# Performance work log

Measured on AMD Instinct MI355X. Metric: run time of the kernel, lower is better.

## Reference

```python
import jax, jax.numpy as jnp
import numpy as np

LN_EPS = 1e-5


def setup_inputs() -> dict:
    key = jax.random.key(0)
    ks = jax.random.split(key, 6)
    B, T, D, E, F = 8, 2048, 1024, 8, 4096
    x = jax.random.normal(ks[0], (B, T, D), dtype=jnp.float32)
    router_w = jax.random.normal(ks[1], (E, D), dtype=jnp.float32) * 0.02
    wfc = jax.random.normal(ks[2], (E, F, D), dtype=jnp.float32) * 0.02
    bfc = jnp.zeros((E, F), dtype=jnp.float32)
    wproj = jax.random.normal(ks[3], (E, D, F), dtype=jnp.float32) * 0.02
    bproj = jnp.zeros((E, D), dtype=jnp.float32)
    ln_g = jnp.ones((D,), dtype=jnp.float32)
    ln_b = jnp.zeros((D,), dtype=jnp.float32)
    return {"x": x, "router_w": router_w, "wfc": wfc, "bfc": bfc,
            "wproj": wproj, "bproj": bproj, "ln_g": ln_g, "ln_b": ln_b,
            "top_k": 2}


def reference(x, router_w, wfc, bfc, wproj, bproj, ln_g, ln_b, top_k):
    # Router: [B,T,E] logits, top-k selection, softmax over the k logits.
    router_logits = jnp.einsum('btd,ed->bte', x, router_w)
    top_vals, top_idx = jax.lax.top_k(router_logits, top_k)   # [B,T,K]
    top_probs = jax.nn.softmax(top_vals, axis=-1)             # [B,T,K]

    E = router_w.shape[0]
    out = jnp.zeros_like(x)
    # Dense-per-expert compute with zero gate for unrouted tokens; identical
    # math to the torch gather/scatter loop (dropout inert in eval).
    for e in range(E):
        gate = jnp.sum(jnp.where(top_idx == e, top_probs, 0.0), axis=-1)  # [B,T]
        h = jax.nn.gelu(jnp.einsum('btd,fd->btf', x, wfc[e]) + bfc[e],
                        approximate=False)
        y = jnp.einsum('btf,df->btd', h, wproj[e]) + bproj[e]
        out = out + y * gate[..., None]

    # LayerNorm over hidden dim
    mu = jnp.mean(out, axis=-1, keepdims=True)
    var = jnp.mean(jnp.square(out - mu), axis=-1, keepdims=True)
    out = (out - mu) * jax.lax.rsqrt(var + LN_EPS) * ln_g + ln_b
    return (out, router_logits)
```

## Files before the change

### kernel.cpp

```cpp
#include <hip/hip_runtime.h>

#define NTOK 16384
#define DDIM 1024
#define FDIM 4096
#define NEXP 8
#define PADPAIRS 33792
#define MAXTILES 264

#define WS_XB      0ull
#define WS_WFCB    33554432ull
#define WS_WPROJB  100663296ull
#define WS_H       167772160ull

typedef short bf16x8 __attribute__((ext_vector_type(8)));
typedef float f32x4 __attribute__((ext_vector_type(4)));

__device__ __forceinline__ unsigned short f2bf(float f) {
    unsigned int u = __float_as_uint(f);
    u += 0x7fffu + ((u >> 16) & 1u);
    return (unsigned short)(u >> 16);
}

__device__ __forceinline__ void gload16(const unsigned short* g, const unsigned short* lds) {
    __builtin_amdgcn_global_load_lds(
        (const __attribute__((address_space(1))) unsigned int*)(unsigned long long)(const void*)g,
        (__attribute__((address_space(3))) unsigned int*)(unsigned int)(unsigned long long)(const void*)lds,
        16, 0, 0);
}

__global__ __launch_bounds__(256) void convert_kernel(const float* __restrict__ src,
                                                      unsigned short* __restrict__ dst) {
    int i = blockIdx.x * 256 + threadIdx.x;
    float4 v = ((const float4*)src)[i];
    ushort4 o;
    o.x = f2bf(v.x); o.y = f2bf(v.y); o.z = f2bf(v.z); o.w = f2bf(v.w);
    ((ushort4*)dst)[i] = o;
}

__global__ __launch_bounds__(256) void router_kernel(const float* __restrict__ x,
                                                     const float* __restrict__ rw,
                                                     unsigned short* __restrict__ xb,
                                                     float* __restrict__ logits,
                                                     int* __restrict__ tok_idx,
                                                     float* __restrict__ tok_gate,
                                                     int* __restrict__ counts) {
    __shared__ float srw[NEXP * DDIM];
    __shared__ int scnt[NEXP];
    int tid = threadIdx.x;
    if (tid < NEXP) scnt[tid] = 0;
    for (int i = tid; i < NEXP * DDIM / 4; i += 256)
        ((float4*)srw)[i] = ((const float4*)rw)[i];
    __syncthreads();

    int wave = tid >> 6, lane = tid & 63;
    const float4* srw4 = (const float4*)srw;

    for (int j = 0; j < 4; j++) {
        int t = blockIdx.x * 16 + wave * 4 + j;
        const float4* xr = (const float4*)(x + (size_t)t * DDIM);
        ushort4* xbr = (ushort4*)(xb + (size_t)t * DDIM);

        float acc[NEXP];
#pragma unroll
        for (int e = 0; e < NEXP; e++) acc[e] = 0.f;

#pragma unroll
        for (int i = 0; i < 4; i++) {
            int k4 = i * 64 + lane;
            float4 xv = xr[k4];
            ushort4 o;
            o.x = f2bf(xv.x); o.y = f2bf(xv.y); o.z = f2bf(xv.z); o.w = f2bf(xv.w);
            xbr[k4] = o;
#pragma unroll
            for (int e = 0; e < NEXP; e++) {
                float4 wv = srw4[e * 256 + k4];
                acc[e] += xv.x * wv.x + xv.y * wv.y + xv.z * wv.z + xv.w * wv.w;
            }
        }
#pragma unroll
        for (int off = 1; off < 64; off <<= 1) {
#pragma unroll
            for (int e = 0; e < NEXP; e++) acc[e] += __shfl_xor(acc[e], off);
        }
        if (lane == 0) {
            float v0 = -1e30f, v1 = -1e30f; int i0 = 0, i1 = 0;
#pragma unroll
            for (int e = 0; e < NEXP; e++) {
                float v = acc[e];
                logits[(size_t)t * NEXP + e] = v;
                if (v > v0)      { v1 = v0; i1 = i0; v0 = v; i0 = e; }
                else if (v > v1) { v1 = v;  i1 = e; }
            }
            float d = __expf(v1 - v0);
            float g0 = 1.f / (1.f + d);
            float g1 = d * g0;
            tok_idx[t * 2 + 0] = i0; tok_idx[t * 2 + 1] = i1;
            tok_gate[t * 2 + 0] = g0; tok_gate[t * 2 + 1] = g1;
            atomicAdd(&scnt[i0], 1);
            atomicAdd(&scnt[i1], 1);
        }
    }
    __syncthreads();
    if (tid < NEXP) atomicAdd(&counts[tid], scnt[tid]);
}

__global__ void seg_plan(const int* __restrict__ counts, int* __restrict__ seg_start,
                         int* __restrict__ tile2e, int* __restrict__ total_tiles,
                         int* __restrict__ pair_token, float* __restrict__ pair_gate) {
    if (threadIdx.x == 0) {
        int cum = 0, tl = 0;
        for (int e = 0; e < NEXP; e++) {
            seg_start[e] = cum;
            int tiles = (counts[e] + 127) >> 7;
            for (int i = 0; i < tiles; i++) tile2e[tl++] = e;
            cum += tiles << 7;
        }
        for (int i = tl; i < MAXTILES; i++) tile2e[i] = -1;
        *total_tiles = tl;
    }
    for (int i = threadIdx.x; i < PADPAIRS; i += 256) {
        pair_token[i] = 0;
        pair_gate[i] = 0.f;
    }
}

__global__ __launch_bounds__(256) void scatter_k(const int* __restrict__ tok_idx,
                                                 const float* __restrict__ tok_gate,
                                                 const int* __restrict__ seg_start,
                                                 int* __restrict__ cursor,
                                                 int* __restrict__ pair_token,
                                                 float* __restrict__ pair_gate) {
    int t = blockIdx.x * 256 + threadIdx.x;
#pragma unroll
    for (int s = 0; s < 2; s++) {
        int e = tok_idx[t * 2 + s];
        int pos = seg_start[e] + atomicAdd(&cursor[e], 1);
        pair_token[pos] = t;
        pair_gate[pos] = tok_gate[t * 2 + s];
    }
}

__global__ __launch_bounds__(256, 3) void gemm1_kernel(const unsigned short* __restrict__ xb,
                                                    const unsigned short* __restrict__ wfcb,
                                                    const float* __restrict__ bfc,
                                                    const int* __restrict__ pair_token,
                                                    const int* __restrict__ tile2e,
                                                    int chunk_base,
                                                    unsigned short* __restrict__ h) {
    int tile = chunk_base + blockIdx.y;
    int e = tile2e[tile];
    if (e < 0) return;
    int ftile = blockIdx.x;

    __shared__ unsigned short sA[128 * 64];
    __shared__ unsigned short sB[128 * 64];

    int tid = threadIdx.x;
    int wave = tid >> 6, lane = tid & 63;
    int lrow = lane >> 3;
    int kblk = (lane & 7) ^ lrow;

    const unsigned short* wB = wfcb + (size_t)e * FDIM * DDIM + (size_t)ftile * 128 * DDIM;
    const unsigned short* aBase[4];
    const unsigned short* bBase[4];
#pragma unroll
    for (int t = 0; t < 4; t++) {
        int row = wave * 32 + t * 8 + lrow;
        aBase[t] = xb + (size_t)pair_token[tile * 128 + row] * DDIM + kblk * 8;
        bBase[t] = wB + (size_t)row * DDIM + kblk * 8;
    }

    f32x4 zero = {0.f, 0.f, 0.f, 0.f};
    f32x4 acc[4][4];
#pragma unroll
    for (int i = 0; i < 4; i++)
#pragma unroll
        for (int j = 0; j < 4; j++) acc[i][j] = zero;

    int wm = (wave >> 1) * 64, wn = (wave & 1) * 64;
    int quad = lane >> 4, l16 = lane & 15;
    int r7 = l16 & 7;

    for (int k0 = 0; k0 < DDIM; k0 += 64) {
#pragma unroll
        for (int t = 0; t < 4; t++) {
            gload16(aBase[t], &sA[(wave * 32 + t * 8) * 64]);
            gload16(bBase[t], &sB[(wave * 32 + t * 8) * 64]);
            aBase[t] += 64; bBase[t] += 64;
        }
        __syncthreads();
#pragma unroll
        for (int ks = 0; ks < 64; ks += 32) {
            int g = (ks >> 3) + quad;
            bf16x8 af[4], bfr[4];
#pragma unroll
            for (int i = 0; i < 4; i++) {
                int row = wm + i * 16 + l16;
                af[i] = *(const bf16x8*)&sA[row * 64 + ((g ^ r7) << 3)];
            }
#pragma unroll
            for (int j = 0; j < 4; j++) {
                int row = wn + j * 16 + l16;
                bfr[j] = *(const bf16x8*)&sB[row * 64 + ((g ^ r7) << 3)];
            }
#pragma unroll
            for (int i = 0; i < 4; i++)
#pragma unroll
                for (int j = 0; j < 4; j++)
                    acc[i][j] = __builtin_amdgcn_mfma_f32_16x16x32_bf16(af[i], bfr[j], acc[i][j], 0, 0, 0);
        }
        __syncthreads();
    }

    unsigned short* hrow_base = h + (size_t)blockIdx.y * 128 * FDIM;
#pragma unroll
    for (int i = 0; i < 4; i++) {
#pragma unroll
        for (int j = 0; j < 4; j++) {
            int col = wn + j * 16 + l16;
            int f = ftile * 128 + col;
            float bias = bfc[e * FDIM + f];
#pragma unroll
            for (int r = 0; r < 4; r++) {
                int row = wm + i * 16 + quad * 4 + r;
                float v = acc[i][j][r] + bias;
                v = 0.5f * v * (1.f + erff(v * 0.70710678118654752f));
                hrow_base[(size_t)row * FDIM + f] = f2bf(v);
            }
        }
    }
}

__global__ __launch_bounds__(256, 3) void gemm2_kernel(const unsigned short* __restrict__ h,
                                                    const unsigned short* __restrict__ wprojb,
                                                    const float* __restrict__ bproj,
                                                    const int* __restrict__ pair_token,
                                                    const float* __restrict__ pair_gate,
                                                    const int* __restrict__ tile2e,
                                                    int chunk_base,
                                                    float* __restrict__ out) {
    int tile = chunk_base + blockIdx.y;
    int e = tile2e[tile];
    if (e < 0) return;
    int dtile = blockIdx.x;

    __shared__ unsigned short sA[128 * 64];
    __shared__ unsigned short sB[128 * 64];

    int tid = threadIdx.x;
    int wave = tid >> 6, lane = tid & 63;
    int lrow = lane >> 3;
    int kblk = (lane & 7) ^ lrow;

    const unsigned short* hA = h + (size_t)blockIdx.y * 128 * FDIM;
    const unsigned short* wB = wprojb + (size_t)e * DDIM * FDIM + (size_t)dtile * 128 * FDIM;
    const unsigned short* aBase[4];
    const unsigned short* bBase[4];
#pragma unroll
    for (int t = 0; t < 4; t++) {
        int row = wave * 32 + t * 8 + lrow;
        aBase[t] = hA + (size_t)row * FDIM + kblk * 8;
        bBase[t] = wB + (size_t)row * FDIM + kblk * 8;
    }

    f32x4 zero = {0.f, 0.f, 0.f, 0.f};
    f32x4 acc[4][4];
#pragma unroll
    for (int i = 0; i < 4; i++)
#pragma unroll
        for (int j = 0; j < 4; j++) acc[i][j] = zero;

    int wm = (wave >> 1) * 64, wn = (wave & 1) * 64;
    int quad = lane >> 4, l16 = lane & 15;
    int r7 = l16 & 7;

    for (int k0 = 0; k0 < FDIM; k0 += 64) {
#pragma unroll
        for (int t = 0; t < 4; t++) {
            gload16(aBase[t], &sA[(wave * 32 + t * 8) * 64]);
            gload16(bBase[t], &sB[(wave * 32 + t * 8) * 64]);
            aBase[t] += 64; bBase[t] += 64;
        }
        __syncthreads();
#pragma unroll
        for (int ks = 0; ks < 64; ks += 32) {
            int g = (ks >> 3) + quad;
            bf16x8 af[4], bfr[4];
#pragma unroll
            for (int i = 0; i < 4; i++) {
                int row = wm + i * 16 + l16;
                af[i] = *(const bf16x8*)&sA[row * 64 + ((g ^ r7) << 3)];
            }
#pragma unroll
            for (int j = 0; j < 4; j++) {
                int row = wn + j * 16 + l16;
                bfr[j] = *(const bf16x8*)&sB[row * 64 + ((g ^ r7) << 3)];
            }
#pragma unroll
            for (int i = 0; i < 4; i++)
#pragma unroll
                for (int j = 0; j < 4; j++)
                    acc[i][j] = __builtin_amdgcn_mfma_f32_16x16x32_bf16(af[i], bfr[j], acc[i][j], 0, 0, 0);
        }
        __syncthreads();
    }

#pragma unroll
    for (int i = 0; i < 4; i++) {
#pragma unroll
        for (int j = 0; j < 4; j++) {
            int col = wn + j * 16 + l16;
            int d = dtile * 128 + col;
            float bias = bproj[e * DDIM + d];
#pragma unroll
            for (int r = 0; r < 4; r++) {
                int row = wm + i * 16 + quad * 4 + r;
                int tok = pair_token[tile * 128 + row];
                float gate = pair_gate[tile * 128 + row];
                float v = (acc[i][j][r] + bias) * gate;
                atomicAdd(&out[(size_t)tok * DDIM + d], v);
            }
        }
    }
}

__global__ __launch_bounds__(256) void ln_kernel(float* __restrict__ out,
                                                 const float* __restrict__ g,
                                                 const float* __restrict__ b) {
    __shared__ float s1[4], s2[4];
    int t = blockIdx.x, tid = threadIdx.x;
    float* row = out + (size_t)t * DDIM;
    float4 v = ((const float4*)row)[tid];
    float sum = v.x + v.y + v.z + v.w;
    float sq = v.x * v.x + v.y * v.y + v.z * v.z + v.w * v.w;
#pragma unroll
    for (int off = 32; off > 0; off >>= 1) {
        sum += __shfl_down(sum, off);
        sq  += __shfl_down(sq, off);
    }
    int wave = tid >> 6, lane = tid & 63;
    if (lane == 0) { s1[wave] = sum; s2[wave] = sq; }
    __syncthreads();
    float tot = s1[0] + s1[1] + s1[2] + s1[3];
    float totsq = s2[0] + s2[1] + s2[2] + s2[3];
    float mu = tot * (1.f / DDIM);
    float var = totsq * (1.f / DDIM) - mu * mu;
    float rs = rsqrtf(var + 1e-5f);
    float4 gv = ((const float4*)g)[tid];
    float4 bv = ((const float4*)b)[tid];
    float4 o;
    o.x = (v.x - mu) * rs * gv.x + bv.x;
    o.y = (v.y - mu) * rs * gv.y + bv.y;
    o.z = (v.z - mu) * rs * gv.z + bv.z;
    o.w = (v.w - mu) * rs * gv.w + bv.w;
    ((float4*)row)[tid] = o;
}

extern "C" void kernel_launch(void* const* d_in, const int* in_sizes, int n_in,
                              void* d_out, int out_size, void* d_ws, size_t ws_size,
                              hipStream_t stream) {
    const float* x   = (const float*)d_in[0];
    const float* rw  = (const float*)d_in[1];
    const float* wfc = (const float*)d_in[2];
    const float* bfc = (const float*)d_in[3];
    const float* wpr = (const float*)d_in[4];
    const float* bpr = (const float*)d_in[5];
    const float* lng = (const float*)d_in[6];
    const float* lnb = (const float*)d_in[7];

    float* out = (float*)d_out;
    float* logits = out + (size_t)NTOK * DDIM;

    char* ws = (char*)d_ws;
    unsigned short* xb     = (unsigned short*)(ws + WS_XB);
    unsigned short* wfcb   = (unsigned short*)(ws + WS_WFCB);
    unsigned short* wprojb = (unsigned short*)(ws + WS_WPROJB);
    unsigned short* hbuf   = (unsigned short*)(ws + WS_H);

    size_t aux_bytes = (size_t)PADPAIRS * 8 + (size_t)NTOK * 16 + 4096;
    int ct = 66;
    if (ws_size >= WS_H + (size_t)264 * 128 * FDIM * 2 + aux_bytes)      ct = 264;
    else if (ws_size >= WS_H + (size_t)132 * 128 * FDIM * 2 + aux_bytes) ct = 132;
    int nchunks = MAXTILES / ct;

    char* aux = ws + WS_H + (size_t)ct * 128 * FDIM * 2;
    int*   ptok  = (int*)aux;
    float* pgate = (float*)(aux + (size_t)PADPAIRS * 4);
    int*   tidx  = (int*)(aux + (size_t)PADPAIRS * 8);
    float* tgate = (float*)(aux + (size_t)PADPAIRS * 8 + (size_t)NTOK * 8);
    int*   meta  = (int*)(aux + (size_t)PADPAIRS * 8 + (size_t)NTOK * 16);
    int* counts = meta;
    int* cursor = meta + 8;
    int* segs   = meta + 16;
    int* total  = meta + 24;
    int* tile2e = meta + 32;

    hipMemsetAsync(out, 0, (size_t)NTOK * DDIM * sizeof(float), stream);
    hipMemsetAsync(meta, 0, 64, stream);

    convert_kernel<<<(NEXP * FDIM * DDIM) / 4 / 256, 256, 0, stream>>>(wfc, wfcb);
    convert_kernel<<<(NEXP * DDIM * FDIM) / 4 / 256, 256, 0, stream>>>(wpr, wprojb);
    router_kernel<<<NTOK / 16, 256, 0, stream>>>(x, rw, xb, logits, tidx, tgate, counts);
    seg_plan<<<1, 256, 0, stream>>>(counts, segs, tile2e, total, ptok, pgate);
    scatter_k<<<NTOK / 256, 256, 0, stream>>>(tidx, tgate, segs, cursor, ptok, pgate);

    for (int c = 0; c < nchunks; c++) {
        gemm1_kernel<<<dim3(FDIM / 128, ct), 256, 0, stream>>>(
            xb, wfcb, bfc, ptok, tile2e, c * ct, hbuf);
        gemm2_kernel<<<dim3(DDIM / 128, ct), 256, 0, stream>>>(
            hbuf, wprojb, bpr, ptok, pgate, tile2e, c * ct, out);
    }
    ln_kernel<<<NTOK, 256, 0, stream>>>(out, lng, lnb);
}
```

Before: 1.343 ms.

## Double-buffer A tiles in expert GEMMs and aggregate scatter atomics per block

Both grouped GEMM kernels now double-buffer the gathered A (token) tile in LDS. The next A tile is prefetched while the current one is consumed, using explicit vmcnt waits and raw s_barrier with sched_barrier fences in place of full __syncthreads. The scatter kernel ranks pairs per block through LDS atomics and issues one global atomic per expert per block, and the expert counters and cursors are padded to separate cache lines. This is meant to hide global-load latency in the GEMM main loops and cut atomic contention, at the cost of extra LDS per block (possible occupancy loss) and more fragile manual waitcnt logic.

```diff
diff --git a/kernel.cpp b/kernel.cpp
--- a/kernel.cpp
+++ b/kernel.cpp
@@ -27,6 +27,8 @@
         (__attribute__((address_space(3))) unsigned int*)(unsigned int)(unsigned long long)(const void*)lds,
         16, 0, 0);
 }
+
+#define SCHED0() __builtin_amdgcn_sched_barrier(0)
 
 __global__ __launch_bounds__(256) void convert_kernel(const float* __restrict__ src,
                                                       unsigned short* __restrict__ dst) {
@@ -101,7 +103,7 @@
         }
     }
     __syncthreads();
-    if (tid < NEXP) atomicAdd(&counts[tid], scnt[tid]);
+    if (tid < NEXP) atomicAdd(&counts[tid * 16], scnt[tid]);
 }
 
 __global__ void seg_plan(const int* __restrict__ counts, int* __restrict__ seg_start,
@@ -111,7 +113,7 @@
         int cum = 0, tl = 0;
         for (int e = 0; e < NEXP; e++) {
             seg_start[e] = cum;
-            int tiles = (counts[e] + 127) >> 7;
+            int tiles = (counts[e * 16] + 127) >> 7;
             for (int i = 0; i < tiles; i++) tile2e[tl++] = e;
             cum += tiles << 7;
         }
@@ -130,14 +132,23 @@
                                                  int* __restrict__ cursor,
                                                  int* __restrict__ pair_token,
                                                  float* __restrict__ pair_gate) {
-    int t = blockIdx.x * 256 + threadIdx.x;
-#pragma unroll
-    for (int s = 0; s < 2; s++) {
-        int e = tok_idx[t * 2 + s];
-        int pos = seg_start[e] + atomicAdd(&cursor[e], 1);
-        pair_token[pos] = t;
-        pair_gate[pos] = tok_gate[t * 2 + s];
-    }
+    __shared__ int lcnt[NEXP];
+    __shared__ int lbase[NEXP];
+    int tid = threadIdx.x;
+    if (tid < NEXP) lcnt[tid] = 0;
+    __syncthreads();
+    int t = blockIdx.x * 256 + tid;
+    int e0 = tok_idx[t * 2 + 0], e1 = tok_idx[t * 2 + 1];
+    float g0 = tok_gate[t * 2 + 0], g1 = tok_gate[t * 2 + 1];
+    int r0 = atomicAdd(&lcnt[e0], 1);
+    int r1 = atomicAdd(&lcnt[e1], 1);
+    __syncthreads();
+    if (tid < NEXP) lbase[tid] = atomicAdd(&cursor[tid * 16], lcnt[tid]);
+    __syncthreads();
+    int p0 = seg_start[e0] + lbase[e0] + r0;
+    int p1 = seg_start[e1] + lbase[e1] + r1;
+    pair_token[p0] = t; pair_gate[p0] = g0;
+    pair_token[p1] = t; pair_gate[p1] = g1;
 }
 
 __global__ __launch_bounds__(256, 3) void gemm1_kernel(const unsigned short* __restrict__ xb,
@@ -152,7 +163,7 @@
     if (e < 0) return;
     int ftile = blockIdx.x;
 
-    __shared__ unsigned short sA[128 * 64];
+    __shared__ unsigned short sA[2][128 * 64];
     __shared__ unsigned short sB[128 * 64];
 
     int tid = threadIdx.x;
@@ -181,14 +192,33 @@
     int quad = lane >> 4, l16 = lane & 15;
     int r7 = l16 & 7;
 
-    for (int k0 = 0; k0 < DDIM; k0 += 64) {
+    constexpr int NK = DDIM / 64;
+#pragma unroll
+    for (int t = 0; t < 4; t++) {
+        gload16(aBase[t], &sA[0][(wave * 32 + t * 8) * 64]);
+        aBase[t] += 64;
+    }
+    SCHED0();
+
+#pragma unroll 1
+    for (int k = 0; k < NK - 1; ++k) {
 #pragma unroll
         for (int t = 0; t < 4; t++) {
-            gload16(aBase[t], &sA[(wave * 32 + t * 8) * 64]);
             gload16(bBase[t], &sB[(wave * 32 + t * 8) * 64]);
-            aBase[t] += 64; bBase[t] += 64;
-        }
-        __syncthreads();
+            bBase[t] += 64;
+        }
+        const unsigned short* sAn = sA[(k + 1) & 1];
+#pragma unroll
+        for (int t = 0; t < 4; t++) {
+            gload16(aBase[t], &sAn[(wave * 32 + t * 8) * 64]);
+            aBase[t] += 64;
+        }
+        SCHED0();
+        asm volatile("s_waitcnt vmcnt(4)" ::: "memory");
+        SCHED0();
+        __builtin_amdgcn_s_barrier();
+        SCHED0();
+        const unsigned short* sAc = sA[k & 1];
 #pragma unroll
         for (int ks = 0; ks < 64; ks += 32) {
             int g = (ks >> 3) + quad;
@@ -196,7 +226,7 @@
 #pragma unroll
             for (int i = 0; i < 4; i++) {
                 int row = wm + i * 16 + l16;
-                af[i] = *(const bf16x8*)&sA[row * 64 + ((g ^ r7) << 3)];
+                af[i] = *(const bf16x8*)&sAc[row * 64 + ((g ^ r7) << 3)];
             }
 #pragma unroll
             for (int j = 0; j < 4; j++) {
@@ -209,7 +239,40 @@
                 for (int j = 0; j < 4; j++)
                     acc[i][j] = __builtin_amdgcn_mfma_f32_16x16x32_bf16(af[i], bfr[j], acc[i][j], 0, 0, 0);
         }
-        __syncthreads();
+        SCHED0();
+        __builtin_amdgcn_s_barrier();
+        SCHED0();
+    }
+    {
+#pragma unroll
+        for (int t = 0; t < 4; t++)
+            gload16(bBase[t], &sB[(wave * 32 + t * 8) * 64]);
+        SCHED0();
+        asm volatile("s_waitcnt vmcnt(0)" ::: "memory");
+        SCHED0();
+        __builtin_amdgcn_s_barrier();
+        SCHED0();
+        const unsigned short* sAc = sA[(NK - 1) & 1];
+#pragma unroll
+        for (int ks = 0; ks < 64; ks += 32) {
+            int g = (ks >> 3) + quad;
+            bf16x8 af[4], bfr[4];
+#pragma unroll
+            for (int i = 0; i < 4; i++) {
+                int row = wm + i * 16 + l16;
+                af[i] = *(const bf16x8*)&sAc[row * 64 + ((g ^ r7) << 3)];
+            }
+#pragma unroll
+            for (int j = 0; j < 4; j++) {
+                int row = wn + j * 16 + l16;
+                bfr[j] = *(const bf16x8*)&sB[row * 64 + ((g ^ r7) << 3)];
+            }
+#pragma unroll
+            for (int i = 0; i < 4; i++)
+#pragma unroll
+                for (int j = 0; j < 4; j++)
+                    acc[i][j] = __builtin_amdgcn_mfma_f32_16x16x32_bf16(af[i], bfr[j], acc[i][j], 0, 0, 0);
+        }
     }
 
     unsigned short* hrow_base = h + (size_t)blockIdx.y * 128 * FDIM;
@@ -244,7 +307,7 @@
     if (e < 0) return;
     int dtile = blockIdx.x;
 
-    __shared__ unsigned short sA[128 * 64];
+    __shared__ unsigned short sA[2][128 * 64];
     __shared__ unsigned short sB[128 * 64];
 
     int tid = threadIdx.x;
@@ -274,14 +337,33 @@
     int quad = lane >> 4, l16 = lane & 15;
     int r7 = l16 & 7;
 
-    for (int k0 = 0; k0 < FDIM; k0 += 64) {
+    constexpr int NK = FDIM / 64;
+#pragma unroll
+    for (int t = 0; t < 4; t++) {
+        gload16(aBase[t], &sA[0][(wave * 32 + t * 8) * 64]);
+        aBase[t] += 64;
+    }
+    SCHED0();
+
+#pragma unroll 1
+    for (int k = 0; k < NK - 1; ++k) {
 #pragma unroll
         for (int t = 0; t < 4; t++) {
-            gload16(aBase[t], &sA[(wave * 32 + t * 8) * 64]);
             gload16(bBase[t], &sB[(wave * 32 + t * 8) * 64]);
-            aBase[t] += 64; bBase[t] += 64;
-        }
-        __syncthreads();
+            bBase[t] += 64;
+        }
+        const unsigned short* sAn = sA[(k + 1) & 1];
+#pragma unroll
+        for (int t = 0; t < 4; t++) {
+            gload16(aBase[t], &sAn[(wave * 32 + t * 8) * 64]);
+            aBase[t] += 64;
+        }
+        SCHED0();
+        asm volatile("s_waitcnt vmcnt(4)" ::: "memory");
+        SCHED0();
+        __builtin_amdgcn_s_barrier();
+        SCHED0();
+        const unsigned short* sAc = sA[k & 1];
 #pragma unroll
         for (int ks = 0; ks < 64; ks += 32) {
             int g = (ks >> 3) + quad;
@@ -289,7 +371,7 @@
 #pragma unroll
             for (int i = 0; i < 4; i++) {
                 int row = wm + i * 16 + l16;
-                af[i] = *(const bf16x8*)&sA[row * 64 + ((g ^ r7) << 3)];
+                af[i] = *(const bf16x8*)&sAc[row * 64 + ((g ^ r7) << 3)];
             }
 #pragma unroll
             for (int j = 0; j < 4; j++) {
@@ -302,7 +384,40 @@
                 for (int j = 0; j < 4; j++)
                     acc[i][j] = __builtin_amdgcn_mfma_f32_16x16x32_bf16(af[i], bfr[j], acc[i][j], 0, 0, 0);
         }
-        __syncthreads();
+        SCHED0();
+        __builtin_amdgcn_s_barrier();
+        SCHED0();
+    }
+    {
+#pragma unroll
+        for (int t = 0; t < 4; t++)
+            gload16(bBase[t], &sB[(wave * 32 + t * 8) * 64]);
+        SCHED0();
+        asm volatile("s_waitcnt vmcnt(0)" ::: "memory");
+        SCHED0();
+        __builtin_amdgcn_s_barrier();
+        SCHED0();
+        const unsigned short* sAc = sA[(NK - 1) & 1];
+#pragma unroll
+        for (int ks = 0; ks < 64; ks += 32) {
+            int g = (ks >> 3) + quad;
+            bf16x8 af[4], bfr[4];
+#pragma unroll
+            for (int i = 0; i < 4; i++) {
+                int row = wm + i * 16 + l16;
+                af[i] = *(const bf16x8*)&sAc[row * 64 + ((g ^ r7) << 3)];
+            }
+#pragma unroll
+            for (int j = 0; j < 4; j++) {
+                int row = wn + j * 16 + l16;
+                bfr[j] = *(const bf16x8*)&sB[row * 64 + ((g ^ r7) << 3)];
+            }
+#pragma unroll
+            for (int i = 0; i < 4; i++)
+#pragma unroll
+                for (int j = 0; j < 4; j++)
+                    acc[i][j] = __builtin_amdgcn_mfma_f32_16x16x32_bf16(af[i], bfr[j], acc[i][j], 0, 0, 0);
+        }
     }
 
 #pragma unroll
@@ -377,7 +492,7 @@
     unsigned short* wprojb = (unsigned short*)(ws + WS_WPROJB);
     unsigned short* hbuf   = (unsigned short*)(ws + WS_H);
 
-    size_t aux_bytes = (size_t)PADPAIRS * 8 + (size_t)NTOK * 16 + 4096;
+    size_t aux_bytes = (size_t)PADPAIRS * 8 + (size_t)NTOK * 16 + 8192;
     int ct = 66;
     if (ws_size >= WS_H + (size_t)264 * 128 * FDIM * 2 + aux_bytes)      ct = 264;
     else if (ws_size >= WS_H + (size_t)132 * 128 * FDIM * 2 + aux_bytes) ct = 132;
@@ -390,13 +505,13 @@
     float* tgate = (float*)(aux + (size_t)PADPAIRS * 8 + (size_t)NTOK * 8);
     int*   meta  = (int*)(aux + (size_t)PADPAIRS * 8 + (size_t)NTOK * 16);
     int* counts = meta;
-    int* cursor = meta + 8;
-    int* segs   = meta + 16;
-    int* total  = meta + 24;
-    int* tile2e = meta + 32;
+    int* cursor = meta + 128;
+    int* segs   = meta + 256;
+    int* total  = meta + 264;
+    int* tile2e = meta + 272;
 
     hipMemsetAsync(out, 0, (size_t)NTOK * DDIM * sizeof(float), stream);
-    hipMemsetAsync(meta, 0, 64, stream);
+    hipMemsetAsync(meta, 0, 2048, stream);
 
     convert_kernel<<<(NEXP * FDIM * DDIM) / 4 / 256, 256, 0, stream>>>(wfc, wfcb);
     convert_kernel<<<(NEXP * DDIM * FDIM) / 4 / 256, 256, 0, stream>>>(wpr, wprojb);
```

Result: faster. 1.165 ms (-13.3%).
